# Optimization experiments

Hardware: AMD Instinct MI355X
Metric: run time of the kernel (lower is better)

Reference implementation:

```python
import jax, jax.numpy as jnp
import numpy as np

N = 50000      # nodes
E = 800000     # edges (avg degree 16)
F_IN = 256
HID = 256
N_CLASSES = 128


def setup_inputs() -> dict:
    key = jax.random.key(0)
    ks = jax.random.split(key, 12)
    x = jax.random.normal(ks[0], (N, F_IN), dtype=jnp.float32)
    src = jax.random.randint(ks[1], (E,), 0, N)
    dst = jax.random.randint(ks[2], (E,), 0, N)
    inp = {"x": x, "src": src, "dst": dst}
    dims = [(F_IN, HID), (HID, HID), (HID, N_CLASSES)]
    for l, (din, dout) in enumerate(dims):
        s = 1.0 / np.sqrt(din)
        inp[f"W_self_{l}"] = jax.random.uniform(ks[3 + 3 * l], (dout, din), jnp.float32, -s, s)
        inp[f"W_neigh_{l}"] = jax.random.uniform(ks[4 + 3 * l], (dout, din), jnp.float32, -s, s)
        inp[f"b_{l}"] = jnp.zeros((dout,), jnp.float32)
    return inp


def _mean_agg(h, src, dst, n):
    # mean over in-neighbors: gather src features, segment-sum into dst, divide by in-degree
    s = jax.ops.segment_sum(h[src], dst, num_segments=n)          # [N, F]
    deg = jax.ops.segment_sum(jnp.ones((src.shape[0],), h.dtype), dst, num_segments=n)
    return s / jnp.maximum(deg, 1.0)[:, None]


def reference(x, W_self_0, W_neigh_0, b_0, W_self_1, W_neigh_1, b_1,
              W_self_2, W_neigh_2, b_2, src, dst):
    # DGL SAGEConv('mean'): out = fc_self(h_dst) + fc_neigh(mean_neigh(h)) + bias
    layers = [(W_self_0, W_neigh_0, b_0),
              (W_self_1, W_neigh_1, b_1),
              (W_self_2, W_neigh_2, b_2)]
    n = x.shape[0]
    h = x
    for l, (Ws, Wn, b) in enumerate(layers):
        agg = _mean_agg(h, src, dst, n)
        h = h @ Ws.T + agg @ Wn.T + b
        if l != len(layers) - 1:
            h = jax.nn.relu(h)  # dropout p=0 -> identity
    return h
```

## Files before the change

### kernel.cpp

```cpp
#include <hip/hip_runtime.h>
#include <stdint.h>

#define NNODES 50000
#define NEDGES 800000
#define NB_SCAN ((NNODES + 255) / 256)
#define NB_CVTX 12500
#define NB_CVTW 384
#define NB_HIST 3125

typedef _Float16 f16;
typedef _Float16 f16x4 __attribute__((ext_vector_type(4)));
typedef _Float16 f16x8 __attribute__((ext_vector_type(8)));
typedef float f32x4 __attribute__((ext_vector_type(4)));
typedef float f32x8 __attribute__((ext_vector_type(8)));

static inline size_t align_up(size_t x, size_t a){ return (x + a - 1) & ~(a - 1); }

__device__ __forceinline__ void gll16(const void* g, void* l){
  __builtin_amdgcn_global_load_lds((const __attribute__((address_space(1))) uint32_t*)(g),
                                   (__attribute__((address_space(3))) uint32_t*)(l), 16, 0, 0);
}

__device__ __forceinline__ f16x8 ld8(const f16* p){ return *reinterpret_cast<const f16x8*>(p); }

__global__ void __launch_bounds__(256) k_pre(const float* __restrict__ x, f16* __restrict__ xh,
                       const float* __restrict__ a0, const float* __restrict__ a1,
                       const float* __restrict__ a2, const float* __restrict__ a3,
                       const float* __restrict__ a4, const float* __restrict__ a5,
                       f16* __restrict__ o0, f16* __restrict__ o1, f16* __restrict__ o2,
                       f16* __restrict__ o3, f16* __restrict__ o4, f16* __restrict__ o5,
                       const int* __restrict__ dst, int* __restrict__ deg){
  int b = blockIdx.x;
  int tid = threadIdx.x;
  if (b < NB_CVTX){
    int i = b * 256 + tid;
    float4 v = *reinterpret_cast<const float4*>(&x[(size_t)i * 4]);
    f16x4 o = { (f16)v.x, (f16)v.y, (f16)v.z, (f16)v.w };
    *reinterpret_cast<f16x4*>(&xh[(size_t)i * 4]) = o;
  } else if (b < NB_CVTX + NB_CVTW){
    int bb = b - NB_CVTX;
    int seg = bb >> 6;
    const float* in; f16* out; int n;
    switch (seg){
      case 0: in = a0; out = o0; n = 65536; break;
      case 1: in = a1; out = o1; n = 65536; break;
      case 2: in = a2; out = o2; n = 65536; break;
      case 3: in = a3; out = o3; n = 65536; break;
      case 4: in = a4; out = o4; n = 32768; break;
      default: in = a5; out = o5; n = 32768; break;
    }
    int i = ((bb & 63) * 256 + tid) * 4;
    if (i < n){
      float4 v = *reinterpret_cast<const float4*>(&in[i]);
      f16x4 o = { (f16)v.x, (f16)v.y, (f16)v.z, (f16)v.w };
      *reinterpret_cast<f16x4*>(&out[i]) = o;
    }
  } else {
    int i = (b - NB_CVTX - NB_CVTW) * 256 + tid;
    if (i < NEDGES) atomicAdd(&deg[dst[i]], 1);
  }
}

__global__ void __launch_bounds__(256) k_scan1(const int* __restrict__ deg,
                        int* __restrict__ row_ptr, int* __restrict__ bsum, int n){
  __shared__ int s[256];
  int tid = threadIdx.x;
  int i = blockIdx.x * 256 + tid;
  int v = (i < n) ? deg[i] : 0;
  s[tid] = v;
  __syncthreads();
  #pragma unroll
  for (int off = 1; off < 256; off <<= 1){
    int t = (tid >= off) ? s[tid - off] : 0;
    __syncthreads();
    s[tid] += t;
    __syncthreads();
  }
  if (i < n) row_ptr[i] = s[tid] - v;
  if (tid == 255) bsum[blockIdx.x] = s[255];
}

__global__ void __launch_bounds__(256) k_scan2(const int* __restrict__ bsum,
                        int* __restrict__ boff, int* __restrict__ row_ptr, int nb, int n){
  __shared__ int s[256];
  int tid = threadIdx.x;
  int v = (tid < nb) ? bsum[tid] : 0;
  s[tid] = v;
  __syncthreads();
  #pragma unroll
  for (int off = 1; off < 256; off <<= 1){
    int t = (tid >= off) ? s[tid - off] : 0;
    __syncthreads();
    s[tid] += t;
    __syncthreads();
  }
  if (tid < nb) boff[tid] = s[tid] - v;
  if (tid == 255) row_ptr[n] = s[255];
}

__global__ void __launch_bounds__(256) k_scan3(int* __restrict__ row_ptr,
                        const int* __restrict__ boff, int* __restrict__ cursor, int n){
  int i = blockIdx.x * 256 + threadIdx.x;
  if (i < n){
    int v = row_ptr[i] + boff[blockIdx.x];
    row_ptr[i] = v;
    cursor[i] = v;
  }
}

__global__ void k_fill(const int* __restrict__ src, const int* __restrict__ dst,
                       int* __restrict__ cursor, int* __restrict__ csr, int e){
  int i = blockIdx.x * blockDim.x + threadIdx.x;
  if (i < e){
    int p = atomicAdd(&cursor[dst[i]], 1);
    csr[p] = src[i];
  }
}

__global__ void __launch_bounds__(256) k_mm(const f16* __restrict__ A,
                                            const f16* __restrict__ Bw,
                                            f16* __restrict__ C, int M, int N){
  __shared__ __align__(16) char sm[65536];
  int nwg = gridDim.x;
  int q = nwg >> 3, r = nwg & 7;
  int xcd = blockIdx.x & 7, seq = blockIdx.x >> 3;
  int t = (xcd < r) ? xcd * (q + 1) + seq : r * (q + 1) + (xcd - r) * q + seq;
  int nbn = N >> 7;
  int mi = t / nbn, ni = t - mi * nbn;
  int m0 = mi * 128, n0 = ni * 128;

  int tid = threadIdx.x;
  int lane = tid & 63, wid = tid >> 6;
  int wm = (wid & 1) * 64, wn = (wid >> 1) * 64;

  f32x4 acc[4][4];
  #pragma unroll
  for (int m = 0; m < 4; ++m)
    #pragma unroll
    for (int n = 0; n < 4; ++n)
      acc[m][n] = (f32x4){0.f, 0.f, 0.f, 0.f};

  const int srow = tid >> 3;
  const int scolx = ((tid & 7) << 4) ^ ((srow & 7) << 4);
  const char* Ab = (const char*)A;
  const char* Bb = (const char*)Bw;

  auto STAGE = [&](int kt, int buf){
    int kbyte = kt * 128;
    char* sA = sm + buf * 16384;
    char* sB = sm + 32768 + buf * 16384;
    #pragma unroll
    for (int qq = 0; qq < 4; ++qq){
      int row = qq * 32 + srow;
      int ga = m0 + row; if (ga >= M) ga = M - 1;
      int gb = n0 + row;
      gll16(Ab + (size_t)ga * 512 + kbyte + scolx, sA + qq * 4096 + wid * 1024);
      gll16(Bb + (size_t)gb * 512 + kbyte + scolx, sB + qq * 4096 + wid * 1024);
    }
  };

  STAGE(0, 0);
  __syncthreads();
  for (int kt = 0; kt < 4; ++kt){
    int buf = kt & 1;
    if (kt < 3) STAGE(kt + 1, buf ^ 1);
    const char* sA = sm + buf * 16384;
    const char* sB = sm + 32768 + buf * 16384;
    #pragma unroll
    for (int kk = 0; kk < 2; ++kk){
      int cb = kk * 64 + ((lane >> 4) << 4);
      f16x8 af[4], bfr[4];
      #pragma unroll
      for (int m = 0; m < 4; ++m){
        int rr = wm + m * 16 + (lane & 15);
        af[m] = *reinterpret_cast<const f16x8*>(sA + rr * 128 + (cb ^ ((rr & 7) << 4)));
      }
      #pragma unroll
      for (int n = 0; n < 4; ++n){
        int rr = wn + n * 16 + (lane & 15);
        bfr[n] = *reinterpret_cast<const f16x8*>(sB + rr * 128 + (cb ^ ((rr & 7) << 4)));
      }
      #pragma unroll
      for (int m = 0; m < 4; ++m)
        #pragma unroll
        for (int n = 0; n < 4; ++n)
          acc[m][n] = __builtin_amdgcn_mfma_f32_16x16x32_f16(af[m], bfr[n], acc[m][n], 0, 0, 0);
    }
    __syncthreads();
  }

  f16* ep = (f16*)(sm + wid * 2304);
  int cl = lane & 15, rq = lane >> 4;
  #pragma unroll
  for (int m = 0; m < 4; ++m){
    #pragma unroll
    for (int n = 0; n < 4; ++n)
      #pragma unroll
      for (int j = 0; j < 4; ++j)
        ep[(rq * 4 + j) * 68 + n * 16 + cl] = (f16)acc[m][n][j];
    #pragma unroll
    for (int pass = 0; pass < 2; ++pass){
      int row = (lane >> 3) + pass * 8;
      int col8 = (lane & 7) * 8;
      f16x8 v = *reinterpret_cast<const f16x8*>(&ep[row * 68 + col8]);
      int gr = m0 + wm + m * 16 + row;
      if (gr < M)
        *reinterpret_cast<f16x8*>(&C[(size_t)gr * N + n0 + wn + col8]) = v;
    }
  }
}

__global__ void __launch_bounds__(256) k_comb(const f16* __restrict__ sp,
                        const int* __restrict__ row_ptr,
                        const int* __restrict__ csr,
                        const float* __restrict__ bias,
                        f16* __restrict__ h){
  int wid = threadIdx.x >> 6, lane = threadIdx.x & 63;
  int node = blockIdx.x * 4 + wid;
  if (node >= NNODES) return;
  int s = row_ptr[node], e = row_ptr[node + 1];
  int hh = lane >> 5, fl = lane & 31;
  const f16* pbase = sp + 256 + (size_t)fl * 8;
  f32x8 accA = {0,0,0,0,0,0,0,0}, accB = {0,0,0,0,0,0,0,0};
  int p = s + hh;
  while (p + 2 < e){
    int j0 = csr[p], j1 = csr[p + 2];
    f16x8 v0 = ld8(pbase + (size_t)j0 * 512);
    f16x8 v1 = ld8(pbase + (size_t)j1 * 512);
    #pragma unroll
    for (int c = 0; c < 8; ++c){ accA[c] += (float)v0[c]; accB[c] += (float)v1[c]; }
    p += 4;
  }
  if (p < e){
    int j = csr[p];
    f16x8 v = ld8(pbase + (size_t)j * 512);
    #pragma unroll
    for (int c = 0; c < 8; ++c) accA[c] += (float)v[c];
  }
  #pragma unroll
  for (int c = 0; c < 8; ++c){
    float t = accA[c] + accB[c];
    accA[c] = t + __shfl_xor(t, 32);
  }
  int d = e - s;
  float inv = (d > 0) ? 1.f / (float)d : 0.f;
  if (lane < 32){
    f16x8 sv = ld8(&sp[(size_t)node * 512 + fl * 8]);
    float4 ba = *reinterpret_cast<const float4*>(&bias[fl * 8]);
    float4 bb = *reinterpret_cast<const float4*>(&bias[fl * 8 + 4]);
    float bv[8] = {ba.x, ba.y, ba.z, ba.w, bb.x, bb.y, bb.z, bb.w};
    f16x8 o;
    #pragma unroll
    for (int c = 0; c < 8; ++c){
      float x = (float)sv[c] + bv[c] + accA[c] * inv;
      o[c] = (f16)fmaxf(x, 0.f);
    }
    *reinterpret_cast<f16x8*>(&h[(size_t)node * 256 + fl * 8]) = o;
  }
}

__global__ void __launch_bounds__(256) k_comb2(const f16* __restrict__ sp,
                        const int* __restrict__ row_ptr,
                        const int* __restrict__ csr,
                        const float* __restrict__ bias,
                        float* __restrict__ out){
  int wid = threadIdx.x >> 6, lane = threadIdx.x & 63;
  int node = blockIdx.x * 4 + wid;
  if (node >= NNODES) return;
  int s = row_ptr[node], e = row_ptr[node + 1];
  int hh = lane >> 4, fl = lane & 15;
  const f16* pbase = sp + 128 + (size_t)fl * 8;
  f32x8 accA = {0,0,0,0,0,0,0,0}, accB = {0,0,0,0,0,0,0,0};
  int p = s + hh;
  while (p + 4 < e){
    int j0 = csr[p], j1 = csr[p + 4];
    f16x8 v0 = ld8(pbase + (size_t)j0 * 256);
    f16x8 v1 = ld8(pbase + (size_t)j1 * 256);
    #pragma unroll
    for (int c = 0; c < 8; ++c){ accA[c] += (float)v0[c]; accB[c] += (float)v1[c]; }
    p += 8;
  }
  if (p < e){
    int j = csr[p];
    f16x8 v = ld8(pbase + (size_t)j * 256);
    #pragma unroll
    for (int c = 0; c < 8; ++c) accA[c] += (float)v[c];
  }
  #pragma unroll
  for (int c = 0; c < 8; ++c){
    float t = accA[c] + accB[c];
    t += __shfl_xor(t, 16);
    accA[c] = t + __shfl_xor(t, 32);
  }
  int d = e - s;
  float inv = (d > 0) ? 1.f / (float)d : 0.f;
  if (lane < 16){
    f16x8 sv = ld8(&sp[(size_t)node * 256 + fl * 8]);
    float4 ba = *reinterpret_cast<const float4*>(&bias[fl * 8]);
    float4 bb = *reinterpret_cast<const float4*>(&bias[fl * 8 + 4]);
    float4 o1, o2;
    o1.x = (float)sv[0] + ba.x + accA[0] * inv;
    o1.y = (float)sv[1] + ba.y + accA[1] * inv;
    o1.z = (float)sv[2] + ba.z + accA[2] * inv;
    o1.w = (float)sv[3] + ba.w + accA[3] * inv;
    o2.x = (float)sv[4] + bb.x + accA[4] * inv;
    o2.y = (float)sv[5] + bb.y + accA[5] * inv;
    o2.z = (float)sv[6] + bb.z + accA[6] * inv;
    o2.w = (float)sv[7] + bb.w + accA[7] * inv;
    *reinterpret_cast<float4*>(&out[(size_t)node * 128 + fl * 8]) = o1;
    *reinterpret_cast<float4*>(&out[(size_t)node * 128 + fl * 8 + 4]) = o2;
  }
}

extern "C" void kernel_launch(void* const* d_in, const int* in_sizes, int n_in,
                              void* d_out, int out_size, void* d_ws, size_t ws_size,
                              hipStream_t stream){
  const float* x   = (const float*)d_in[0];
  const int*   src = (const int*)d_in[1];
  const int*   dst = (const int*)d_in[2];
  const float* Ws0 = (const float*)d_in[3];
  const float* Wn0 = (const float*)d_in[4];
  const float* b0  = (const float*)d_in[5];
  const float* Ws1 = (const float*)d_in[6];
  const float* Wn1 = (const float*)d_in[7];
  const float* b1  = (const float*)d_in[8];
  const float* Ws2 = (const float*)d_in[9];
  const float* Wn2 = (const float*)d_in[10];
  const float* b2  = (const float*)d_in[11];
  float* out = (float*)d_out;

  char* ws = (char*)d_ws;
  size_t off = 0;
  int* deg     = (int*)(ws + off); off = align_up(off + (size_t)NNODES * 4, 256);
  int* row_ptr = (int*)(ws + off); off = align_up(off + (size_t)(NNODES + 1) * 4, 256);
  int* cursor  = (int*)(ws + off); off = align_up(off + (size_t)NNODES * 4, 256);
  int* csr     = (int*)(ws + off); off = align_up(off + (size_t)NEDGES * 4, 256);
  int* bsum    = (int*)(ws + off); off = align_up(off + (size_t)256 * 4, 256);
  int* boff    = (int*)(ws + off); off = align_up(off + (size_t)256 * 4, 256);
  f16* xh   = (f16*)(ws + off); off = align_up(off + (size_t)NNODES * 256 * 2, 256);
  f16* hA   = (f16*)(ws + off); off = align_up(off + (size_t)NNODES * 256 * 2, 256);
  f16* sp   = (f16*)(ws + off); off = align_up(off + (size_t)NNODES * 512 * 2, 256);
  f16* w16  = (f16*)(ws + off); off = align_up(off + (size_t)327680 * 2, 256);
  f16* Ws0h = w16;              f16* Wn0h = w16 + 65536;
  f16* Ws1h = w16 + 131072;     f16* Wn1h = w16 + 196608;
  f16* Ws2h = w16 + 262144;     f16* Wn2h = w16 + 294912;
  f16* hB = xh;
  (void)ws_size; (void)in_sizes; (void)n_in; (void)out_size;

  hipMemsetAsync(deg, 0, (size_t)NNODES * 4, stream);
  k_pre<<<NB_CVTX + NB_CVTW + NB_HIST, 256, 0, stream>>>(
      x, xh, Ws0, Wn0, Ws1, Wn1, Ws2, Wn2,
      Ws0h, Wn0h, Ws1h, Wn1h, Ws2h, Wn2h, dst, deg);
  k_scan1<<<NB_SCAN, 256, 0, stream>>>(deg, row_ptr, bsum, NNODES);
  k_scan2<<<1, 256, 0, stream>>>(bsum, boff, row_ptr, NB_SCAN, NNODES);
  k_scan3<<<NB_SCAN, 256, 0, stream>>>(row_ptr, boff, cursor, NNODES);
  k_fill<<<(NEDGES + 255) / 256, 256, 0, stream>>>(src, dst, cursor, csr, NEDGES);

  int gm = (NNODES + 127) / 128;
  int gc = (NNODES + 3) / 4;
  k_mm<<<gm * 4, 256, 0, stream>>>(xh, Ws0h, sp, NNODES, 512);
  k_comb<<<gc, 256, 0, stream>>>(sp, row_ptr, csr, b0, hA);
  k_mm<<<gm * 4, 256, 0, stream>>>(hA, Ws1h, sp, NNODES, 512);
  k_comb<<<gc, 256, 0, stream>>>(sp, row_ptr, csr, b1, hB);
  k_mm<<<gm * 2, 256, 0, stream>>>(hB, Ws2h, sp, NNODES, 256);
  k_comb2<<<gc, 256, 0, stream>>>(sp, row_ptr, csr, b2, out);
}
```

Baseline: 327.6 us.

## Fuse x fp32-to-fp16 conversion into first GEMM, merge scan kernels, split aggregation by feature chunk

The first GEMM now reads fp32 x directly, converting to fp16 in registers and writing the result to LDS. This removes the separate conversion pass and the fp16 copy of x. The two scan kernels are merged by having each block redo the small block-sum scan itself. The aggregation kernels now use two blocks per node group, each covering half of the feature columns, with more edges processed in parallel per wave, which doubles the grid. The fp32 A path goes through registers instead of direct-to-LDS loads, which adds register pressure and ALU work in the first GEMM.

```diff
diff --git a/kernel.cpp b/kernel.cpp
--- a/kernel.cpp
+++ b/kernel.cpp
@@ -4,7 +4,6 @@
 #define NNODES 50000
 #define NEDGES 800000
 #define NB_SCAN ((NNODES + 255) / 256)
-#define NB_CVTX 12500
 #define NB_CVTW 384
 #define NB_HIST 3125
 
@@ -23,7 +22,7 @@
 
 __device__ __forceinline__ f16x8 ld8(const f16* p){ return *reinterpret_cast<const f16x8*>(p); }
 
-__global__ void __launch_bounds__(256) k_pre(const float* __restrict__ x, f16* __restrict__ xh,
+__global__ void __launch_bounds__(256) k_pre(
                        const float* __restrict__ a0, const float* __restrict__ a1,
                        const float* __restrict__ a2, const float* __restrict__ a3,
                        const float* __restrict__ a4, const float* __restrict__ a5,
@@ -32,14 +31,8 @@
                        const int* __restrict__ dst, int* __restrict__ deg){
   int b = blockIdx.x;
   int tid = threadIdx.x;
-  if (b < NB_CVTX){
-    int i = b * 256 + tid;
-    float4 v = *reinterpret_cast<const float4*>(&x[(size_t)i * 4]);
-    f16x4 o = { (f16)v.x, (f16)v.y, (f16)v.z, (f16)v.w };
-    *reinterpret_cast<f16x4*>(&xh[(size_t)i * 4]) = o;
-  } else if (b < NB_CVTX + NB_CVTW){
-    int bb = b - NB_CVTX;
-    int seg = bb >> 6;
+  if (b < NB_CVTW){
+    int seg = b >> 6;
     const float* in; f16* out; int n;
     switch (seg){
       case 0: in = a0; out = o0; n = 65536; break;
@@ -49,14 +42,14 @@
       case 4: in = a4; out = o4; n = 32768; break;
       default: in = a5; out = o5; n = 32768; break;
     }
-    int i = ((bb & 63) * 256 + tid) * 4;
+    int i = ((b & 63) * 256 + tid) * 4;
     if (i < n){
       float4 v = *reinterpret_cast<const float4*>(&in[i]);
       f16x4 o = { (f16)v.x, (f16)v.y, (f16)v.z, (f16)v.w };
       *reinterpret_cast<f16x4*>(&out[i]) = o;
     }
   } else {
-    int i = (b - NB_CVTX - NB_CVTW) * 256 + tid;
+    int i = (b - NB_CVTW) * 256 + tid;
     if (i < NEDGES) atomicAdd(&deg[dst[i]], 1);
   }
 }
@@ -80,11 +73,12 @@
   if (tid == 255) bsum[blockIdx.x] = s[255];
 }
 
-__global__ void __launch_bounds__(256) k_scan2(const int* __restrict__ bsum,
-                        int* __restrict__ boff, int* __restrict__ row_ptr, int nb, int n){
+__global__ void __launch_bounds__(256) k_scan23(const int* __restrict__ bsum,
+                        int* __restrict__ row_ptr, int* __restrict__ cursor, int n){
   __shared__ int s[256];
+  __shared__ int boff_s, tot_s;
   int tid = threadIdx.x;
-  int v = (tid < nb) ? bsum[tid] : 0;
+  int v = (tid < NB_SCAN) ? bsum[tid] : 0;
   s[tid] = v;
   __syncthreads();
   #pragma unroll
@@ -94,18 +88,16 @@
     s[tid] += t;
     __syncthreads();
   }
-  if (tid < nb) boff[tid] = s[tid] - v;
-  if (tid == 255) row_ptr[n] = s[255];
-}
-
-__global__ void __launch_bounds__(256) k_scan3(int* __restrict__ row_ptr,
-                        const int* __restrict__ boff, int* __restrict__ cursor, int n){
-  int i = blockIdx.x * 256 + threadIdx.x;
+  if (tid == (int)blockIdx.x) boff_s = s[tid] - v;
+  if (tid == NB_SCAN - 1) tot_s = s[tid];
+  __syncthreads();
+  int i = blockIdx.x * 256 + tid;
   if (i < n){
-    int v = row_ptr[i] + boff[blockIdx.x];
-    row_ptr[i] = v;
-    cursor[i] = v;
-  }
+    int r = row_ptr[i] + boff_s;
+    row_ptr[i] = r;
+    cursor[i] = r;
+  }
+  if (blockIdx.x == 0 && tid == 0) row_ptr[n] = tot_s;
 }
 
 __global__ void k_fill(const int* __restrict__ src, const int* __restrict__ dst,
@@ -117,7 +109,8 @@
   }
 }
 
-__global__ void __launch_bounds__(256) k_mm(const f16* __restrict__ A,
+template<int AFP32>
+__global__ void __launch_bounds__(256) k_mm(const void* __restrict__ Ain,
                                             const f16* __restrict__ Bw,
                                             f16* __restrict__ C, int M, int N){
   __shared__ __align__(16) char sm[65536];
@@ -142,28 +135,67 @@
 
   const int srow = tid >> 3;
   const int scolx = ((tid & 7) << 4) ^ ((srow & 7) << 4);
-  const char* Ab = (const char*)A;
+  const f16* A16 = (const f16*)Ain;
+  const float* A32 = (const float*)Ain;
+  const char* Ab = (const char*)Ain;
   const char* Bb = (const char*)Bw;
 
-  auto STAGE = [&](int kt, int buf){
+  float4 areg[8];
+  const int arow32 = tid >> 1;
+  const int acol32 = (tid & 1) * 32;
+
+  auto LOADA32 = [&](int kt){
+    int ga = m0 + arow32; if (ga >= M) ga = M - 1;
+    const float* srcp = A32 + (size_t)ga * 256 + kt * 64 + acol32;
+    #pragma unroll
+    for (int qq = 0; qq < 8; ++qq)
+      areg[qq] = *reinterpret_cast<const float4*>(srcp + qq * 4);
+  };
+  auto WRITEA32 = [&](int buf){
+    char* sA = sm + buf * 16384;
+    #pragma unroll
+    for (int j = 0; j < 4; ++j){
+      int c = (tid & 1) * 4 + j;
+      float4 a = areg[2 * j], b = areg[2 * j + 1];
+      f16x8 v = { (f16)a.x, (f16)a.y, (f16)a.z, (f16)a.w,
+                  (f16)b.x, (f16)b.y, (f16)b.z, (f16)b.w };
+      *reinterpret_cast<f16x8*>(sA + arow32 * 128 + ((c * 16) ^ ((arow32 & 7) << 4))) = v;
+    }
+  };
+  auto STAGEA16 = [&](int kt, int buf){
     int kbyte = kt * 128;
     char* sA = sm + buf * 16384;
-    char* sB = sm + 32768 + buf * 16384;
     #pragma unroll
     for (int qq = 0; qq < 4; ++qq){
       int row = qq * 32 + srow;
       int ga = m0 + row; if (ga >= M) ga = M - 1;
+      gll16(Ab + (size_t)ga * 512 + kbyte + scolx, sA + qq * 4096 + wid * 1024);
+    }
+  };
+  auto STAGEB = [&](int kt, int buf){
+    int kbyte = kt * 128;
+    char* sB = sm + 32768 + buf * 16384;
+    #pragma unroll
+    for (int qq = 0; qq < 4; ++qq){
+      int row = qq * 32 + srow;
       int gb = n0 + row;
-      gll16(Ab + (size_t)ga * 512 + kbyte + scolx, sA + qq * 4096 + wid * 1024);
       gll16(Bb + (size_t)gb * 512 + kbyte + scolx, sB + qq * 4096 + wid * 1024);
     }
   };
 
-  STAGE(0, 0);
+  if constexpr (AFP32){
+    LOADA32(0); WRITEA32(0); STAGEB(0, 0);
+  } else {
+    STAGEA16(0, 0); STAGEB(0, 0);
+  }
   __syncthreads();
   for (int kt = 0; kt < 4; ++kt){
     int buf = kt & 1;
-    if (kt < 3) STAGE(kt + 1, buf ^ 1);
+    if (kt < 3){
+      if constexpr (AFP32) LOADA32(kt + 1);
+      else STAGEA16(kt + 1, buf ^ 1);
+      STAGEB(kt + 1, buf ^ 1);
+    }
     const char* sA = sm + buf * 16384;
     const char* sB = sm + 32768 + buf * 16384;
     #pragma unroll
@@ -186,6 +218,7 @@
         for (int n = 0; n < 4; ++n)
           acc[m][n] = __builtin_amdgcn_mfma_f32_16x16x32_f16(af[m], bfr[n], acc[m][n], 0, 0, 0);
     }
+    if constexpr (AFP32){ if (kt < 3) WRITEA32(buf ^ 1); }
     __syncthreads();
   }
 
@@ -215,21 +248,24 @@
                         const int* __restrict__ csr,
                         const float* __restrict__ bias,
                         f16* __restrict__ h){
+  int chunk = blockIdx.x & 1;
+  int grp = blockIdx.x >> 1;
   int wid = threadIdx.x >> 6, lane = threadIdx.x & 63;
-  int node = blockIdx.x * 4 + wid;
+  int node = grp * 4 + wid;
   if (node >= NNODES) return;
   int s = row_ptr[node], e = row_ptr[node + 1];
-  int hh = lane >> 5, fl = lane & 31;
-  const f16* pbase = sp + 256 + (size_t)fl * 8;
+  int qw = lane >> 4, fl = lane & 15;
+  const int fo = chunk * 128 + fl * 8;
+  const f16* pbase = sp + 256 + fo;
   f32x8 accA = {0,0,0,0,0,0,0,0}, accB = {0,0,0,0,0,0,0,0};
-  int p = s + hh;
-  while (p + 2 < e){
-    int j0 = csr[p], j1 = csr[p + 2];
+  int p = s + qw;
+  while (p + 4 < e){
+    int j0 = csr[p], j1 = csr[p + 4];
     f16x8 v0 = ld8(pbase + (size_t)j0 * 512);
     f16x8 v1 = ld8(pbase + (size_t)j1 * 512);
     #pragma unroll
     for (int c = 0; c < 8; ++c){ accA[c] += (float)v0[c]; accB[c] += (float)v1[c]; }
-    p += 4;
+    p += 8;
   }
   if (p < e){
     int j = csr[p];
@@ -240,14 +276,15 @@
   #pragma unroll
   for (int c = 0; c < 8; ++c){
     float t = accA[c] + accB[c];
+    t += __shfl_xor(t, 16);
     accA[c] = t + __shfl_xor(t, 32);
   }
   int d = e - s;
   float inv = (d > 0) ? 1.f / (float)d : 0.f;
-  if (lane < 32){
-    f16x8 sv = ld8(&sp[(size_t)node * 512 + fl * 8]);
-    float4 ba = *reinterpret_cast<const float4*>(&bias[fl * 8]);
-    float4 bb = *reinterpret_cast<const float4*>(&bias[fl * 8 + 4]);
+  if (lane < 16){
+    f16x8 sv = ld8(&sp[(size_t)node * 512 + fo]);
+    float4 ba = *reinterpret_cast<const float4*>(&bias[fo]);
+    float4 bb = *reinterpret_cast<const float4*>(&bias[fo + 4]);
     float bv[8] = {ba.x, ba.y, ba.z, ba.w, bb.x, bb.y, bb.z, bb.w};
     f16x8 o;
     #pragma unroll
@@ -255,7 +292,7 @@
       float x = (float)sv[c] + bv[c] + accA[c] * inv;
       o[c] = (f16)fmaxf(x, 0.f);
     }
-    *reinterpret_cast<f16x8*>(&h[(size_t)node * 256 + fl * 8]) = o;
+    *reinterpret_cast<f16x8*>(&h[(size_t)node * 256 + fo]) = o;
   }
 }
 
@@ -264,21 +301,24 @@
                         const int* __restrict__ csr,
                         const float* __restrict__ bias,
                         float* __restrict__ out){
+  int chunk = blockIdx.x & 1;
+  int grp = blockIdx.x >> 1;
   int wid = threadIdx.x >> 6, lane = threadIdx.x & 63;
-  int node = blockIdx.x * 4 + wid;
+  int node = grp * 4 + wid;
   if (node >= NNODES) return;
   int s = row_ptr[node], e = row_ptr[node + 1];
-  int hh = lane >> 4, fl = lane & 15;
-  const f16* pbase = sp + 128 + (size_t)fl * 8;
+  int ew = lane >> 3, fl = lane & 7;
+  const int fo = chunk * 64 + fl * 8;
+  const f16* pbase = sp + 128 + fo;
   f32x8 accA = {0,0,0,0,0,0,0,0}, accB = {0,0,0,0,0,0,0,0};
-  int p = s + hh;
-  while (p + 4 < e){
-    int j0 = csr[p], j1 = csr[p + 4];
+  int p = s + ew;
+  while (p + 8 < e){
+    int j0 = csr[p], j1 = csr[p + 8];
     f16x8 v0 = ld8(pbase + (size_t)j0 * 256);
     f16x8 v1 = ld8(pbase + (size_t)j1 * 256);
     #pragma unroll
     for (int c = 0; c < 8; ++c){ accA[c] += (float)v0[c]; accB[c] += (float)v1[c]; }
-    p += 8;
+    p += 16;
   }
   if (p < e){
     int j = csr[p];
@@ -289,15 +329,16 @@
   #pragma unroll
   for (int c = 0; c < 8; ++c){
     float t = accA[c] + accB[c];
+    t += __shfl_xor(t, 8);
     t += __shfl_xor(t, 16);
     accA[c] = t + __shfl_xor(t, 32);
   }
   int d = e - s;
   float inv = (d > 0) ? 1.f / (float)d : 0.f;
-  if (lane < 16){
-    f16x8 sv = ld8(&sp[(size_t)node * 256 + fl * 8]);
-    float4 ba = *reinterpret_cast<const float4*>(&bias[fl * 8]);
-    float4 bb = *reinterpret_cast<const float4*>(&bias[fl * 8 + 4]);
+  if (lane < 8){
+    f16x8 sv = ld8(&sp[(size_t)node * 256 + fo]);
+    float4 ba = *reinterpret_cast<const float4*>(&bias[fo]);
+    float4 bb = *reinterpret_cast<const float4*>(&bias[fo + 4]);
     float4 o1, o2;
     o1.x = (float)sv[0] + ba.x + accA[0] * inv;
     o1.y = (float)sv[1] + ba.y + accA[1] * inv;
@@ -307,8 +348,8 @@
     o2.y = (float)sv[5] + bb.y + accA[5] * inv;
     o2.z = (float)sv[6] + bb.z + accA[6] * inv;
     o2.w = (float)sv[7] + bb.w + accA[7] * inv;
-    *reinterpret_cast<float4*>(&out[(size_t)node * 128 + fl * 8]) = o1;
-    *reinterpret_cast<float4*>(&out[(size_t)node * 128 + fl * 8 + 4]) = o2;
+    *reinterpret_cast<float4*>(&out[(size_t)node * 128 + fo]) = o1;
+    *reinterpret_cast<float4*>(&out[(size_t)node * 128 + fo + 4]) = o2;
   }
 }
 
@@ -336,32 +377,29 @@
   int* cursor  = (int*)(ws + off); off = align_up(off + (size_t)NNODES * 4, 256);
   int* csr     = (int*)(ws + off); off = align_up(off + (size_t)NEDGES * 4, 256);
   int* bsum    = (int*)(ws + off); off = align_up(off + (size_t)256 * 4, 256);
-  int* boff    = (int*)(ws + off); off = align_up(off + (size_t)256 * 4, 256);
-  f16* xh   = (f16*)(ws + off); off = align_up(off + (size_t)NNODES * 256 * 2, 256);
   f16* hA   = (f16*)(ws + off); off = align_up(off + (size_t)NNODES * 256 * 2, 256);
+  f16* hB   = (f16*)(ws + off); off = align_up(off + (size_t)NNODES * 256 * 2, 256);
   f16* sp   = (f16*)(ws + off); off = align_up(off + (size_t)NNODES * 512 * 2, 256);
   f16* w16  = (f16*)(ws + off); off = align_up(off + (size_t)327680 * 2, 256);
   f16* Ws0h = w16;              f16* Wn0h = w16 + 65536;
   f16* Ws1h = w16 + 131072;     f16* Wn1h = w16 + 196608;
   f16* Ws2h = w16 + 262144;     f16* Wn2h = w16 + 294912;
-  f16* hB = xh;
   (void)ws_size; (void)in_sizes; (void)n_in; (void)out_size;
 
   hipMemsetAsync(deg, 0, (size_t)NNODES * 4, stream);
-  k_pre<<<NB_CVTX + NB_CVTW + NB_HIST, 256, 0, stream>>>(
-      x, xh, Ws0, Wn0, Ws1, Wn1, Ws2, Wn2,
+  k_pre<<<NB_CVTW + NB_HIST, 256, 0, stream>>>(
+      Ws0, Wn0, Ws1, Wn1, Ws2, Wn2,
       Ws0h, Wn0h, Ws1h, Wn1h, Ws2h, Wn2h, dst, deg);
   k_scan1<<<NB_SCAN, 256, 0, stream>>>(deg, row_ptr, bsum, NNODES);
-  k_scan2<<<1, 256, 0, stream>>>(bsum, boff, row_ptr, NB_SCAN, NNODES);
-  k_scan3<<<NB_SCAN, 256, 0, stream>>>(row_ptr, boff, cursor, NNODES);
+  k_scan23<<<NB_SCAN, 256, 0, stream>>>(bsum, row_ptr, cursor, NNODES);
   k_fill<<<(NEDGES + 255) / 256, 256, 0, stream>>>(src, dst, cursor, csr, NEDGES);
 
   int gm = (NNODES + 127) / 128;
-  int gc = (NNODES + 3) / 4;
-  k_mm<<<gm * 4, 256, 0, stream>>>(xh, Ws0h, sp, NNODES, 512);
+  int gc = ((NNODES + 3) / 4) * 2;
+  k_mm<1><<<gm * 4, 256, 0, stream>>>(x, Ws0h, sp, NNODES, 512);
   k_comb<<<gc, 256, 0, stream>>>(sp, row_ptr, csr, b0, hA);
-  k_mm<<<gm * 4, 256, 0, stream>>>(hA, Ws1h, sp, NNODES, 512);
+  k_mm<0><<<gm * 4, 256, 0, stream>>>(hA, Ws1h, sp, NNODES, 512);
   k_comb<<<gc, 256, 0, stream>>>(sp, row_ptr, csr, b1, hB);
-  k_mm<<<gm * 2, 256, 0, stream>>>(hB, Ws2h, sp, NNODES, 256);
+  k_mm<0><<<gm * 2, 256, 0, stream>>>(hB, Ws2h, sp, NNODES, 256);
   k_comb2<<<gc, 256, 0, stream>>>(sp, row_ptr, csr, b2, out);
 }
```

Measured after the change: 358.4 us. 1.09x slower.
